# Optimization experiments

Measured on AMD Instinct MI355X. Metric: run time of the kernel, lower is better.

The kernel has to match this reference:

```python
import jax, jax.numpy as jnp
import numpy as np

B, T = 1, 1024
HIDDEN = 5376
N_HEADS = 32
N_KV = 4
HEAD_DIM = 512          # global_head_dim (full-attention layer)
ROT_DIM = 128           # head_dim * full_partial_rotary_factor (0.25)
MAX_SEQ = 4096
THETA = 1000000.0       # full_rope_theta
EPS = 1e-6


def _precompute_freqs(rot_dim, max_seq, theta, freq_base_dim):
    # freq exponent uses full head_dim (freq_base_dim) for partial rotary
    freqs = 1.0 / (theta ** (np.arange(0, rot_dim, 2, dtype=np.float32) / freq_base_dim))
    t = np.arange(max_seq, dtype=np.float32)
    ang = np.outer(t, freqs)                      # [max_seq, rot_dim//2]
    return jnp.asarray(np.cos(ang)), jnp.asarray(np.sin(ang))


def setup_inputs() -> dict:
    key = jax.random.key(0)
    ks = jax.random.split(key, 6)
    x = jax.random.normal(ks[0], (B, T, HIDDEN), jnp.float32)
    wq = jax.random.normal(ks[1], (HIDDEN, N_HEADS * HEAD_DIM), jnp.float32) * 0.02
    wk = jax.random.normal(ks[2], (HIDDEN, N_KV * HEAD_DIM), jnp.float32) * 0.02
    wo = jax.random.normal(ks[3], (N_HEADS * HEAD_DIM, HIDDEN), jnp.float32) * 0.02
    q_norm_w = 1.0 + 0.01 * jax.random.normal(ks[4], (HEAD_DIM,), jnp.float32)
    k_norm_w = 1.0 + 0.01 * jax.random.normal(ks[5], (HEAD_DIM,), jnp.float32)
    input_pos = jnp.arange(T, dtype=jnp.int32)    # prefill positions 0..T-1
    # causal mask over the full cache length: key slot s visible iff s <= query pos
    attn_mask = (jnp.arange(MAX_SEQ)[None, :] <= input_pos[:, None])[None, None]  # [1,1,T,S] bool
    fc, fs = _precompute_freqs(ROT_DIM, MAX_SEQ, THETA, HEAD_DIM)
    k_cache = jnp.zeros((B, N_KV, MAX_SEQ, HEAD_DIM), jnp.float32)
    v_cache = jnp.zeros_like(k_cache)
    return dict(x=x, input_pos=input_pos, attn_mask=attn_mask, wq=wq, wk=wk, wo=wo,
                q_norm_w=q_norm_w, k_norm_w=k_norm_w, k_cache=k_cache, v_cache=v_cache,
                freqs_cos=fc, freqs_sin=fs)


def _rmsnorm(x, w=None):
    y = x * jax.lax.rsqrt(jnp.mean(x * x, axis=-1, keepdims=True) + EPS)
    return y * w if w is not None else y


def _rope(t, cos, sin):
    # t: (B,H,T,D); rotate only the first ROT_DIM dims (interleaved pairs), pass the rest
    rot, pas = t[..., :ROT_DIM], t[..., ROT_DIM:]
    r = rot.reshape(rot.shape[:-1] + (ROT_DIM // 2, 2))
    tr, ti = r[..., 0], r[..., 1]
    c = cos[None, None]  # (1,1,T,ROT_DIM//2)
    s = sin[None, None]
    out = jnp.stack([tr * c - ti * s, tr * s + ti * c], axis=-1).reshape(rot.shape)
    return jnp.concatenate([out, pas], axis=-1)


def reference(x, input_pos, attn_mask, wq, wk, wo, q_norm_w, k_norm_w,
              k_cache, v_cache, freqs_cos, freqs_sin):
    q = (x @ wq).reshape(B, T, N_HEADS, HEAD_DIM)
    raw_k = (x @ wk).reshape(B, T, N_KV, HEAD_DIM)   # k_eq_v: raw_v = raw_k
    q = _rmsnorm(q, q_norm_w)
    k = _rmsnorm(raw_k, k_norm_w)
    v = _rmsnorm(raw_k)                               # RMSNormNoWeight on shared K=V
    q = q.transpose(0, 2, 1, 3)                       # (B,H,T,D)
    k = k.transpose(0, 2, 1, 3)
    v = v.transpose(0, 2, 1, 3)
    cos = freqs_cos[input_pos]
    sin = freqs_sin[input_pos]
    q = _rope(q, cos, sin)
    k = _rope(k, cos, sin)
    # KV cache update (index_copy along seq dim)
    k_cache = k_cache.at[:, :, input_pos, :].set(k)
    v_cache = v_cache.at[:, :, input_pos, :].set(v)
    # GQA SDPA with scale=1.0, grouped to avoid materializing repeated K/V
    G = N_HEADS // N_KV
    qg = q.reshape(B, N_KV, G, T, HEAD_DIM)
    scores = jnp.einsum('bkgtd,bksd->bkgts', qg, k_cache)
    neg = jnp.finfo(scores.dtype).min
    scores = jnp.where(attn_mask[:, :, None], scores, neg)  # (1,1,1,T,S) broadcast
    attn = jax.nn.softmax(scores, axis=-1)
    y = jnp.einsum('bkgts,bksd->bkgtd', attn, v_cache).reshape(B, N_HEADS, T, HEAD_DIM)
    y = y.transpose(0, 2, 1, 3).reshape(B, T, N_HEADS * HEAD_DIM)
    return y @ wo
```

## Files before the change

### kernel.cpp

```cpp
#include <hip/hip_runtime.h>
#include <stdint.h>

typedef unsigned short u16;
typedef _Float16 f16;
typedef f16 f16x8 __attribute__((ext_vector_type(8)));
typedef float f32x4 __attribute__((ext_vector_type(4)));
typedef unsigned short u16x4 __attribute__((ext_vector_type(4)));
typedef unsigned short u16x8 __attribute__((ext_vector_type(8)));

#define MFMA16(a, b, c) __builtin_amdgcn_mfma_f32_16x16x32_f16(a, b, c, 0, 0, 0)

__device__ __forceinline__ u16 f2h_u(float f) {
  union { f16 h; u16 u; } v; v.h = (f16)f; return v.u;
}
__device__ __forceinline__ float h2f(u16 u) {
  union { u16 u; f16 h; } v; v.u = u; return (float)v.h;
}
__device__ __forceinline__ f16x8 ld_h8(const u16* p) {
  return *(const f16x8*)p;
}
__device__ __forceinline__ void gl_lds16(const u16* g, u16* l) {
  __builtin_amdgcn_global_load_lds(
      (const __attribute__((address_space(1))) void*)g,
      (__attribute__((address_space(3))) void*)l, 16, 0, 0);
}

__global__ __launch_bounds__(256) void convert_f32_f16(
    const float* __restrict__ in, u16* __restrict__ out, int n8)
{
  int i = blockIdx.x * 256 + threadIdx.x;
  int stride = gridDim.x * 256;
  for (; i < n8; i += stride) {
    f32x4 a = *(const f32x4*)(in + (size_t)i * 8);
    f32x4 b = *(const f32x4*)(in + (size_t)i * 8 + 4);
    u16x8 o;
#pragma unroll
    for (int j = 0; j < 4; ++j) { o[j] = f2h_u(a[j]); o[4 + j] = f2h_u(b[j]); }
    *(u16x8*)(out + (size_t)i * 8) = o;
  }
}

__global__ __launch_bounds__(256) void transpose_h16(
    const u16* __restrict__ in, u16* __restrict__ out,
    int R, int C, int ldi, int ldo, long zin, long zout)
{
  __shared__ u16 tile[64 * 66];
  const u16* ip = in + (size_t)blockIdx.z * zin;
  u16* op = out + (size_t)blockIdx.z * zout;
  int x0 = blockIdx.x * 64, y0 = blockIdx.y * 64;
  int t = threadIdx.x;
  int xr = (t & 15) * 4;
  int yr = t >> 4;
#pragma unroll
  for (int p = 0; p < 4; ++p) {
    int y = yr + p * 16;
    u16x4 v = *(const u16x4*)(ip + (size_t)(y0 + y) * ldi + x0 + xr);
    tile[y * 66 + xr + 0] = v.x;
    tile[y * 66 + xr + 1] = v.y;
    tile[y * 66 + xr + 2] = v.z;
    tile[y * 66 + xr + 3] = v.w;
  }
  __syncthreads();
#pragma unroll
  for (int p = 0; p < 4; ++p) {
    int x = (t >> 4) + p * 16;
    int yq = (t & 15) * 4;
    u16x4 v;
    v.x = tile[(yq + 0) * 66 + x];
    v.y = tile[(yq + 1) * 66 + x];
    v.z = tile[(yq + 2) * 66 + x];
    v.w = tile[(yq + 3) * 66 + x];
    *(u16x4*)(op + (size_t)(x0 + x) * ldo + y0 + yq) = v;
  }
}

template <bool F32OUT>
__global__ __launch_bounds__(512, 4) void gemm_ktn(
    const u16* __restrict__ A, const float* __restrict__ W, void* __restrict__ Cv,
    int Ksp, int lda, int ldw, int ldc, long zstride)
{
  __shared__ alignas(16) u16 As[3 * 256 * 32];
  __shared__ alignas(16) u16 Bs[3 * 128 * 32];
  int tid = threadIdx.x;
  int lane = tid & 63;
  int wave = tid >> 6;
  int wm = wave >> 2, wn = wave & 3;
  int r15 = lane & 15, g = lane >> 4;

  int gx = gridDim.x, gy = gridDim.y;
  int nwg = gx * gy;
  int flat = blockIdx.y * gx + blockIdx.x;
  int q = nwg >> 3, rr = nwg & 7, xcd = flat & 7, lo = flat >> 3;
  int s = ((xcd < rr) ? xcd * (q + 1) : rr * (q + 1) + (xcd - rr) * q) + lo;
  int by = s % gy;
  int bx = s / gy;
  int row0 = by * 256, col0 = bx * 128;
  int kbeg = blockIdx.z * Ksp;

  int rA = tid >> 2;
  int pc = tid & 3;
  int cs = pc ^ ((rA >> 1) & 3);
  const u16* Ag0 = A + (size_t)(row0 + rA) * lda + kbeg + cs * 8;
  const u16* Ag1 = Ag0 + (size_t)128 * lda;

  int cB = tid & 127;
  int kc = tid >> 7;
  const float* Wg = W + (size_t)(kbeg + kc * 8) * ldw + col0 + cB;
  int bwoff = cB * 32 + ((kc ^ ((cB >> 1) & 3)) * 8);

  f32x4 acc[8][2];
#pragma unroll
  for (int i = 0; i < 8; ++i)
#pragma unroll
    for (int j = 0; j < 2; ++j) acc[i][j] = (f32x4){0.f, 0.f, 0.f, 0.f};

  int nk = Ksp >> 5;
  float bw[8];

  auto BLOAD = [&](int kk) {
#pragma unroll
    for (int j = 0; j < 8; ++j)
      bw[j] = Wg[(size_t)(kk * 32 + j) * ldw];
  };
  auto BWRITE = [&](int b) {
    u16x8 o;
#pragma unroll
    for (int j = 0; j < 8; ++j) o[j] = f2h_u(bw[j]);
    *(u16x8*)(Bs + b * 4096 + bwoff) = o;
  };
  auto STAGE_A = [&](int kk, int b) {
    u16* la = As + b * 8192 + wave * 512;
    gl_lds16(Ag0 + (size_t)kk * 32, la);
    gl_lds16(Ag1 + (size_t)kk * 32, la + 4096);
  };

  BLOAD(0);
  STAGE_A(0, 0);
  STAGE_A(1, 1);
  asm volatile("s_waitcnt vmcnt(2)" ::: "memory");
  BWRITE(0);
  asm volatile("s_waitcnt lgkmcnt(0)" ::: "memory");
  __builtin_amdgcn_s_barrier();

  int swz = (g ^ ((r15 >> 1) & 3)) * 8;
  int b0 = 0;
  for (int k = 0; k < nk; ++k) {
    const u16* Ab = As + b0 * 8192;
    const u16* Bb = Bs + b0 * 4096;
    if (k + 1 < nk) BLOAD(k + 1);
    if (k + 2 < nk) {
      int b2 = b0 + 2; if (b2 >= 3) b2 -= 3;
      STAGE_A(k + 2, b2);
    }
    f16x8 bfr[2], af[4];
#pragma unroll
    for (int ni = 0; ni < 2; ++ni)
      bfr[ni] = ld_h8(Bb + (wn * 32 + ni * 16 + r15) * 32 + swz);
#pragma unroll
    for (int m2 = 0; m2 < 4; ++m2)
      af[m2] = ld_h8(Ab + (wm * 128 + m2 * 16 + r15) * 32 + swz);
    __builtin_amdgcn_s_setprio(1);
#pragma unroll
    for (int m2 = 0; m2 < 4; ++m2)
#pragma unroll
      for (int ni = 0; ni < 2; ++ni)
        acc[m2][ni] = MFMA16(af[m2], bfr[ni], acc[m2][ni]);
    f16x8 ag[4];
#pragma unroll
    for (int m2 = 0; m2 < 4; ++m2)
      ag[m2] = ld_h8(Ab + (wm * 128 + (4 + m2) * 16 + r15) * 32 + swz);
#pragma unroll
    for (int m2 = 0; m2 < 4; ++m2)
#pragma unroll
      for (int ni = 0; ni < 2; ++ni)
        acc[4 + m2][ni] = MFMA16(ag[m2], bfr[ni], acc[4 + m2][ni]);
    __builtin_amdgcn_s_setprio(0);
    if (k + 1 < nk) {
      if (k + 2 < nk) {
        asm volatile("s_waitcnt vmcnt(2)" ::: "memory");
      } else {
        asm volatile("s_waitcnt vmcnt(0)" ::: "memory");
      }
      int b1 = b0 + 1; if (b1 >= 3) b1 -= 3;
      BWRITE(b1);
    }
    asm volatile("s_waitcnt lgkmcnt(0)" ::: "memory");
    __builtin_amdgcn_s_barrier();
    b0 = (b0 == 2) ? 0 : b0 + 1;
  }

#pragma unroll
  for (int mi = 0; mi < 8; ++mi)
#pragma unroll
    for (int ni = 0; ni < 2; ++ni) {
      int row = row0 + wm * 128 + mi * 16 + g * 4;
      int col = col0 + wn * 32 + ni * 16 + r15;
#pragma unroll
      for (int r = 0; r < 4; ++r) {
        if constexpr (F32OUT)
          ((float*)Cv)[(size_t)blockIdx.z * zstride + (size_t)(row + r) * ldc + col] = acc[mi][ni][r];
        else
          ((u16*)Cv)[(size_t)blockIdx.z * zstride + (size_t)(row + r) * ldc + col] = f2h_u(acc[mi][ni][r]);
      }
    }
}

__global__ __launch_bounds__(256) void reduce_add2_f32(
    const float* __restrict__ p, float* __restrict__ out, int n4, long half)
{
  int i = blockIdx.x * 256 + threadIdx.x;
  int stride = gridDim.x * 256;
  for (; i < n4; i += stride) {
    f32x4 a = *(const f32x4*)(p + (size_t)i * 4);
    f32x4 b = *(const f32x4*)(p + half + (size_t)i * 4);
    *(f32x4*)(out + (size_t)i * 4) = a + b;
  }
}

__global__ __launch_bounds__(256) void reduce_add4_f16(
    const float* __restrict__ p, u16* __restrict__ out, int n4, long zs)
{
  int i = blockIdx.x * 256 + threadIdx.x;
  int stride = gridDim.x * 256;
  for (; i < n4; i += stride) {
    f32x4 a = *(const f32x4*)(p + (size_t)i * 4);
    a += *(const f32x4*)(p + zs + (size_t)i * 4);
    a += *(const f32x4*)(p + 2 * zs + (size_t)i * 4);
    a += *(const f32x4*)(p + 3 * zs + (size_t)i * 4);
    u16x4 o;
#pragma unroll
    for (int j = 0; j < 4; ++j) o[j] = f2h_u(a[j]);
    *(u16x4*)(out + (size_t)i * 4) = o;
  }
}

__global__ __launch_bounds__(64) void norm_rope_q(
    u16* __restrict__ q, const float* __restrict__ w,
    const float* __restrict__ fc, const float* __restrict__ fs)
{
  int t = blockIdx.x, h = blockIdx.y, lane = threadIdx.x;
  u16* row = q + (size_t)t * 16384 + h * 512;
  u16x8 v = *(const u16x8*)(row + lane * 8);
  float x[8];
  float ss = 0.f;
#pragma unroll
  for (int j = 0; j < 8; ++j) { x[j] = h2f(v[j]); ss += x[j] * x[j]; }
#pragma unroll
  for (int m = 1; m < 64; m <<= 1) ss += __shfl_xor(ss, m, 64);
  float rms = rsqrtf(ss * (1.f / 512.f) + 1e-6f);
  f32x4 w0 = *(const f32x4*)(w + lane * 8);
  f32x4 w1 = *(const f32x4*)(w + lane * 8 + 4);
  float y[8];
#pragma unroll
  for (int j = 0; j < 4; ++j) {
    y[j] = x[j] * rms * w0[j];
    y[4 + j] = x[4 + j] * rms * w1[j];
  }
  if (lane < 16) {
    f32x4 cv = *(const f32x4*)(fc + t * 64 + lane * 4);
    f32x4 sv = *(const f32x4*)(fs + t * 64 + lane * 4);
#pragma unroll
    for (int j = 0; j < 4; ++j) {
      float c = cv[j], s = sv[j];
      float a = y[2 * j], b = y[2 * j + 1];
      y[2 * j] = a * c - b * s;
      y[2 * j + 1] = a * s + b * c;
    }
  }
  u16x8 o;
#pragma unroll
  for (int j = 0; j < 8; ++j) o[j] = f2h_u(y[j]);
  *(u16x8*)(row + lane * 8) = o;
}

__global__ __launch_bounds__(64) void norm_kv(
    u16* __restrict__ kraw, u16* __restrict__ vout, const float* __restrict__ kw,
    const float* __restrict__ fc, const float* __restrict__ fs)
{
  int t = blockIdx.x, kv = blockIdx.y, lane = threadIdx.x;
  u16* row  = kraw + (size_t)t * 2048 + kv * 512;
  u16* vrow = vout + (size_t)t * 2048 + kv * 512;
  u16x8 v = *(const u16x8*)(row + lane * 8);
  float x[8];
  float ss = 0.f;
#pragma unroll
  for (int j = 0; j < 8; ++j) { x[j] = h2f(v[j]); ss += x[j] * x[j]; }
#pragma unroll
  for (int m = 1; m < 64; m <<= 1) ss += __shfl_xor(ss, m, 64);
  float rms = rsqrtf(ss * (1.f / 512.f) + 1e-6f);
  f32x4 w0 = *(const f32x4*)(kw + lane * 8);
  f32x4 w1 = *(const f32x4*)(kw + lane * 8 + 4);
  float yk[8], yv[8];
#pragma unroll
  for (int j = 0; j < 4; ++j) {
    yv[j] = x[j] * rms;           yv[4 + j] = x[4 + j] * rms;
    yk[j] = yv[j] * w0[j];        yk[4 + j] = yv[4 + j] * w1[j];
  }
  if (lane < 16) {
    f32x4 cv = *(const f32x4*)(fc + t * 64 + lane * 4);
    f32x4 sv = *(const f32x4*)(fs + t * 64 + lane * 4);
#pragma unroll
    for (int j = 0; j < 4; ++j) {
      float c = cv[j], s = sv[j];
      float a = yk[2 * j], b = yk[2 * j + 1];
      yk[2 * j] = a * c - b * s;
      yk[2 * j + 1] = a * s + b * c;
    }
  }
  u16x8 ok, ov;
#pragma unroll
  for (int j = 0; j < 8; ++j) { ok[j] = f2h_u(yk[j]); ov[j] = f2h_u(yv[j]); }
  *(u16x8*)(row + lane * 8) = ok;
  *(u16x8*)(vrow + lane * 8) = ov;
}

__global__ __launch_bounds__(256) void attn2_kernel(
    const u16* __restrict__ Q, const u16* __restrict__ Kb,
    const u16* __restrict__ Vt, u16* __restrict__ Y)
{
  __shared__ float Sred[4 * 32 * 68];
  __shared__ u16 Plds[32 * 64];
  __shared__ float scf[32];
  __shared__ float linv[32];
  __shared__ int nf[4];

  int h = blockIdx.x;
  int qtb = 31 - blockIdx.y;
  int kv = h >> 3;
  int tid = threadIdx.x;
  int lane = tid & 63;
  int w = tid >> 6;
  int r15 = lane & 15, g = lane >> 4;
  int qbase = qtb * 32;
  int dbase = w * 128;

  int jloc = lane >> 3, cl = lane & 7;
  int jrow = w * 8 + jloc;
  int qr_sm = qbase + jrow;

  f16x8 qf[2][4];
  {
    const u16* qp = Q + (size_t)(qbase + r15) * 16384 + h * 512 + dbase + g * 8;
#pragma unroll
    for (int mi = 0; mi < 2; ++mi)
#pragma unroll
      for (int ks = 0; ks < 4; ++ks)
        qf[mi][ks] = ld_h8(qp + (size_t)mi * 16 * 16384 + ks * 32);
  }

  f32x4 acc[2][8];
#pragma unroll
  for (int mi = 0; mi < 2; ++mi)
#pragma unroll
    for (int nt = 0; nt < 8; ++nt) acc[mi][nt] = (f32x4){0.f, 0.f, 0.f, 0.f};
  float m_ = -1e30f, l_ = 0.f;

  const u16* kp_base = Kb + kv * 512 + dbase;
  const u16* vt_base = Vt + (size_t)kv * (512 * 1024) + (size_t)dbase * 1024;
  int nst = (qbase + 31) / 64 + 1;

  for (int st = 0; st < nst; ++st) {
    int s0 = st * 64;
    f32x4 sa[2][4];
#pragma unroll
    for (int mi = 0; mi < 2; ++mi)
#pragma unroll
      for (int nt = 0; nt < 4; ++nt) sa[mi][nt] = (f32x4){0.f, 0.f, 0.f, 0.f};
#pragma unroll
    for (int ks = 0; ks < 4; ++ks) {
#pragma unroll
      for (int nt = 0; nt < 4; ++nt) {
        f16x8 kf = ld_h8(kp_base + (size_t)(s0 + nt * 16 + r15) * 2048 + ks * 32 + g * 8);
#pragma unroll
        for (int mi = 0; mi < 2; ++mi)
          sa[mi][nt] = MFMA16(qf[mi][ks], kf, sa[mi][nt]);
      }
    }
    {
      float* sw = Sred + w * 32 * 68;
#pragma unroll
      for (int mi = 0; mi < 2; ++mi)
#pragma unroll
        for (int nt = 0; nt < 4; ++nt)
#pragma unroll
          for (int r = 0; r < 4; ++r)
            sw[(mi * 16 + g * 4 + r) * 68 + nt * 16 + r15] = sa[mi][nt][r];
    }
    __syncthreads();

    {
      const float* sp = Sred + jrow * 68 + cl * 8;
      f32x4 a0 = *(const f32x4*)(sp);
      f32x4 a1 = *(const f32x4*)(sp + 4);
#pragma unroll
      for (int p = 1; p < 4; ++p) {
        a0 += *(const f32x4*)(sp + p * 32 * 68);
        a1 += *(const f32x4*)(sp + p * 32 * 68 + 4);
      }
      float sv[8];
      int sbase = s0 + cl * 8;
#pragma unroll
      for (int j = 0; j < 4; ++j) {
        sv[j]     = (sbase + j     <= qr_sm) ? a0[j] : -1e30f;
        sv[4 + j] = (sbase + 4 + j <= qr_sm) ? a1[j] : -1e30f;
      }
      float mm = sv[0];
#pragma unroll
      for (int j = 1; j < 8; ++j) mm = fmaxf(mm, sv[j]);
      mm = fmaxf(mm, __shfl_xor(mm, 1, 64));
      mm = fmaxf(mm, __shfl_xor(mm, 2, 64));
      mm = fmaxf(mm, __shfl_xor(mm, 4, 64));
      bool defer = (mm <= m_ + 8.f);
      float sc;
      if (defer) { sc = 1.f; }
      else { float mn = fmaxf(m_, mm); sc = __expf(m_ - mn); m_ = mn; }
      float pv8[8], rsum = 0.f;
#pragma unroll
      for (int j = 0; j < 8; ++j) { pv8[j] = __expf(sv[j] - m_); rsum += pv8[j]; }
      rsum += __shfl_xor(rsum, 1, 64);
      rsum += __shfl_xor(rsum, 2, 64);
      rsum += __shfl_xor(rsum, 4, 64);
      l_ = l_ * sc + rsum;
      u16x8 pw;
#pragma unroll
      for (int j = 0; j < 8; ++j) pw[j] = f2h_u(pv8[j]);
      *(u16x8*)(Plds + jrow * 64 + ((cl ^ (jrow & 7)) * 8)) = pw;
      if (cl == 0) scf[jrow] = sc;
      int need = __any((int)(!defer));
      if (lane == 0) nf[w] = need;
    }
    __syncthreads();

    if (nf[0] | nf[1] | nf[2] | nf[3]) {
#pragma unroll
      for (int mi = 0; mi < 2; ++mi)
#pragma unroll
        for (int r = 0; r < 4; ++r) {
          float s = scf[mi * 16 + g * 4 + r];
#pragma unroll
          for (int nt = 0; nt < 8; ++nt) acc[mi][nt][r] *= s;
        }
    }
    f16x8 pa[2][2];
#pragma unroll
    for (int mi = 0; mi < 2; ++mi)
#pragma unroll
      for (int ks = 0; ks < 2; ++ks) {
        int row = mi * 16 + r15;
        int c = ks * 4 + g;
        pa[mi][ks] = ld_h8(Plds + row * 64 + ((c ^ (row & 7)) * 8));
      }
#pragma unroll
    for (int ks = 0; ks < 2; ++ks)
#pragma unroll
      for (int nt = 0; nt < 8; ++nt) {
        f16x8 vf = ld_h8(vt_base + (size_t)(nt * 16 + r15) * 1024 + s0 + ks * 32 + g * 8);
#pragma unroll
        for (int mi = 0; mi < 2; ++mi)
          acc[mi][nt] = MFMA16(pa[mi][ks], vf, acc[mi][nt]);
      }
  }

  if (cl == 0) linv[jrow] = 1.0f / l_;
  __syncthreads();
#pragma unroll
  for (int mi = 0; mi < 2; ++mi)
#pragma unroll
    for (int r = 0; r < 4; ++r) {
      int row = mi * 16 + g * 4 + r;
      float li = linv[row];
      u16* yp = Y + (size_t)(qbase + row) * 16384 + h * 512 + dbase + r15;
#pragma unroll
      for (int nt = 0; nt < 8; ++nt)
        yp[nt * 16] = f2h_u(acc[mi][nt][r] * li);
    }
}

extern "C" void kernel_launch(void* const* d_in, const int* in_sizes, int n_in,
                              void* d_out, int out_size, void* d_ws, size_t ws_size,
                              hipStream_t stream)
{
  const float* x  = (const float*)d_in[0];
  const float* wq = (const float*)d_in[3];
  const float* wk = (const float*)d_in[4];
  const float* wo = (const float*)d_in[5];
  const float* qw = (const float*)d_in[6];
  const float* kw = (const float*)d_in[7];
  const float* fc = (const float*)d_in[10];
  const float* fs = (const float*)d_in[11];
  float* out = (float*)d_out;
  char* ws = (char*)d_ws;

  u16* Qbuf = (u16*)(ws + 0);
  u16* Kbuf = (u16*)(ws + 33554432);
  u16* Vbuf = (u16*)(ws + 37748736);
  u16* Vt   = (u16*)(ws + 41943040);
  u16* Ybuf = (u16*)(ws + 46137344);
  u16* xh   = (u16*)(ws + 79691776);
  float* Pb  = (float*)ws;
  float* PbK = (float*)(ws + 46137344);

  convert_f32_f16<<<672, 256, 0, stream>>>(x, xh, (1024 * 5376) / 8);

  gemm_ktn<false><<<dim3(128, 4, 1), 512, 0, stream>>>(
      xh, wq, (void*)Qbuf, 5376, 5376, 16384, 16384, 0L);

  gemm_ktn<true><<<dim3(16, 4, 4), 512, 0, stream>>>(
      xh, wk, (void*)PbK, 1344, 5376, 2048, 2048, 2097152L);
  reduce_add4_f16<<<2048, 256, 0, stream>>>(PbK, Kbuf, 524288, 2097152L);

  norm_rope_q<<<dim3(1024, 32), 64, 0, stream>>>(Qbuf, qw, fc, fs);
  norm_kv<<<dim3(1024, 4), 64, 0, stream>>>(Kbuf, Vbuf, kw, fc, fs);
  transpose_h16<<<dim3(8, 16, 4), 256, 0, stream>>>(
      Vbuf, Vt, 1024, 512, 2048, 1024, 512L, 524288L);
  attn2_kernel<<<dim3(32, 32), 256, 0, stream>>>(Qbuf, Kbuf, Vt, Ybuf);

  gemm_ktn<true><<<dim3(42, 4, 2), 512, 0, stream>>>(
      Ybuf, wo, (void*)Pb, 8192, 16384, 5376, 5376, 5505024L);
  reduce_add2_f32<<<2048, 256, 0, stream>>>(Pb, out, 1376256, 5505024L);
}
```

Baseline: 853.5 us.

## Double-buffer W register prefetch two k-steps ahead in GEMM main loop

```diff
diff --git a/kernel.cpp b/kernel.cpp
--- a/kernel.cpp
+++ b/kernel.cpp
@@ -115,79 +115,126 @@
     for (int j = 0; j < 2; ++j) acc[i][j] = (f32x4){0.f, 0.f, 0.f, 0.f};
 
   int nk = Ksp >> 5;
-  float bw[8];
-
-  auto BLOAD = [&](int kk) {
-#pragma unroll
-    for (int j = 0; j < 8; ++j)
-      bw[j] = Wg[(size_t)(kk * 32 + j) * ldw];
-  };
-  auto BWRITE = [&](int b) {
-    u16x8 o;
-#pragma unroll
-    for (int j = 0; j < 8; ++j) o[j] = f2h_u(bw[j]);
-    *(u16x8*)(Bs + b * 4096 + bwoff) = o;
-  };
+  float bw0[8], bw1[8];
+
   auto STAGE_A = [&](int kk, int b) {
     u16* la = As + b * 8192 + wave * 512;
     gl_lds16(Ag0 + (size_t)kk * 32, la);
     gl_lds16(Ag1 + (size_t)kk * 32, la + 4096);
   };
-
-  BLOAD(0);
+  int swz = (g ^ ((r15 >> 1) & 3)) * 8;
+
+#define BLOAD0(kk) { _Pragma("unroll") for (int j = 0; j < 8; ++j) bw0[j] = Wg[(size_t)((kk) * 32 + j) * ldw]; }
+#define BLOAD1(kk) { _Pragma("unroll") for (int j = 0; j < 8; ++j) bw1[j] = Wg[(size_t)((kk) * 32 + j) * ldw]; }
+#define BWRITE0(b) { u16x8 o; _Pragma("unroll") for (int j = 0; j < 8; ++j) o[j] = f2h_u(bw0[j]); *(u16x8*)(Bs + (b) * 4096 + bwoff) = o; }
+#define BWRITE1(b) { u16x8 o; _Pragma("unroll") for (int j = 0; j < 8; ++j) o[j] = f2h_u(bw1[j]); *(u16x8*)(Bs + (b) * 4096 + bwoff) = o; }
+
+  BLOAD0(0);
+  BLOAD1(1);
   STAGE_A(0, 0);
   STAGE_A(1, 1);
   asm volatile("s_waitcnt vmcnt(2)" ::: "memory");
-  BWRITE(0);
+  BWRITE0(0);
   asm volatile("s_waitcnt lgkmcnt(0)" ::: "memory");
   __builtin_amdgcn_s_barrier();
 
-  int swz = (g ^ ((r15 >> 1) & 3)) * 8;
   int b0 = 0;
-  for (int k = 0; k < nk; ++k) {
-    const u16* Ab = As + b0 * 8192;
-    const u16* Bb = Bs + b0 * 4096;
-    if (k + 1 < nk) BLOAD(k + 1);
-    if (k + 2 < nk) {
-      int b2 = b0 + 2; if (b2 >= 3) b2 -= 3;
-      STAGE_A(k + 2, b2);
-    }
-    f16x8 bfr[2], af[4];
-#pragma unroll
-    for (int ni = 0; ni < 2; ++ni)
-      bfr[ni] = ld_h8(Bb + (wn * 32 + ni * 16 + r15) * 32 + swz);
-#pragma unroll
-    for (int m2 = 0; m2 < 4; ++m2)
-      af[m2] = ld_h8(Ab + (wm * 128 + m2 * 16 + r15) * 32 + swz);
-    __builtin_amdgcn_s_setprio(1);
-#pragma unroll
-    for (int m2 = 0; m2 < 4; ++m2)
+  for (int k = 0; k < nk; k += 2) {
+    {
+      const int t = k;
+      const u16* Ab = As + b0 * 8192;
+      const u16* Bb = Bs + b0 * 4096;
+      if (t + 2 < nk) {
+        BLOAD0(t + 2);
+        int b2 = b0 + 2; if (b2 >= 3) b2 -= 3;
+        STAGE_A(t + 2, b2);
+      }
+      f16x8 bfr[2], af[4];
 #pragma unroll
       for (int ni = 0; ni < 2; ++ni)
-        acc[m2][ni] = MFMA16(af[m2], bfr[ni], acc[m2][ni]);
-    f16x8 ag[4];
-#pragma unroll
-    for (int m2 = 0; m2 < 4; ++m2)
-      ag[m2] = ld_h8(Ab + (wm * 128 + (4 + m2) * 16 + r15) * 32 + swz);
-#pragma unroll
-    for (int m2 = 0; m2 < 4; ++m2)
-#pragma unroll
-      for (int ni = 0; ni < 2; ++ni)
-        acc[4 + m2][ni] = MFMA16(ag[m2], bfr[ni], acc[4 + m2][ni]);
-    __builtin_amdgcn_s_setprio(0);
-    if (k + 1 < nk) {
-      if (k + 2 < nk) {
-        asm volatile("s_waitcnt vmcnt(2)" ::: "memory");
+        bfr[ni] = ld_h8(Bb + (wn * 32 + ni * 16 + r15) * 32 + swz);
+#pragma unroll
+      for (int m2 = 0; m2 < 4; ++m2)
+        af[m2] = ld_h8(Ab + (wm * 128 + m2 * 16 + r15) * 32 + swz);
+      __builtin_amdgcn_s_setprio(1);
+#pragma unroll
+      for (int m2 = 0; m2 < 4; ++m2)
+#pragma unroll
+        for (int ni = 0; ni < 2; ++ni)
+          acc[m2][ni] = MFMA16(af[m2], bfr[ni], acc[m2][ni]);
+      f16x8 ag[4];
+#pragma unroll
+      for (int m2 = 0; m2 < 4; ++m2)
+        ag[m2] = ld_h8(Ab + (wm * 128 + (4 + m2) * 16 + r15) * 32 + swz);
+#pragma unroll
+      for (int m2 = 0; m2 < 4; ++m2)
+#pragma unroll
+        for (int ni = 0; ni < 2; ++ni)
+          acc[4 + m2][ni] = MFMA16(ag[m2], bfr[ni], acc[4 + m2][ni]);
+      __builtin_amdgcn_s_setprio(0);
+      if (t + 2 < nk) {
+        asm volatile("s_waitcnt vmcnt(10)" ::: "memory");
       } else {
         asm volatile("s_waitcnt vmcnt(0)" ::: "memory");
       }
       int b1 = b0 + 1; if (b1 >= 3) b1 -= 3;
-      BWRITE(b1);
-    }
-    asm volatile("s_waitcnt lgkmcnt(0)" ::: "memory");
-    __builtin_amdgcn_s_barrier();
-    b0 = (b0 == 2) ? 0 : b0 + 1;
-  }
+      BWRITE1(b1);
+      asm volatile("s_waitcnt lgkmcnt(0)" ::: "memory");
+      __builtin_amdgcn_s_barrier();
+      b0 = (b0 == 2) ? 0 : b0 + 1;
+    }
+    {
+      const int t = k + 1;
+      const u16* Ab = As + b0 * 8192;
+      const u16* Bb = Bs + b0 * 4096;
+      if (t + 2 < nk) {
+        BLOAD1(t + 2);
+        int b2 = b0 + 2; if (b2 >= 3) b2 -= 3;
+        STAGE_A(t + 2, b2);
+      }
+      f16x8 bfr[2], af[4];
+#pragma unroll
+      for (int ni = 0; ni < 2; ++ni)
+        bfr[ni] = ld_h8(Bb + (wn * 32 + ni * 16 + r15) * 32 + swz);
+#pragma unroll
+      for (int m2 = 0; m2 < 4; ++m2)
+        af[m2] = ld_h8(Ab + (wm * 128 + m2 * 16 + r15) * 32 + swz);
+      __builtin_amdgcn_s_setprio(1);
+#pragma unroll
+      for (int m2 = 0; m2 < 4; ++m2)
+#pragma unroll
+        for (int ni = 0; ni < 2; ++ni)
+          acc[m2][ni] = MFMA16(af[m2], bfr[ni], acc[m2][ni]);
+      f16x8 ag[4];
+#pragma unroll
+      for (int m2 = 0; m2 < 4; ++m2)
+        ag[m2] = ld_h8(Ab + (wm * 128 + (4 + m2) * 16 + r15) * 32 + swz);
+#pragma unroll
+      for (int m2 = 0; m2 < 4; ++m2)
+#pragma unroll
+        for (int ni = 0; ni < 2; ++ni)
+          acc[4 + m2][ni] = MFMA16(ag[m2], bfr[ni], acc[4 + m2][ni]);
+      __builtin_amdgcn_s_setprio(0);
+      if (t + 1 < nk) {
+        if (t + 2 < nk) {
+          asm volatile("s_waitcnt vmcnt(10)" ::: "memory");
+        } else {
+          asm volatile("s_waitcnt vmcnt(0)" ::: "memory");
+        }
+        int b1 = b0 + 1; if (b1 >= 3) b1 -= 3;
+        BWRITE0(b1);
+      } else {
+        asm volatile("s_waitcnt vmcnt(0)" ::: "memory");
+      }
+      asm volatile("s_waitcnt lgkmcnt(0)" ::: "memory");
+      __builtin_amdgcn_s_barrier();
+      b0 = (b0 == 2) ? 0 : b0 + 1;
+    }
+  }
+#undef BLOAD0
+#undef BLOAD1
+#undef BWRITE0
+#undef BWRITE1
 
 #pragma unroll
   for (int mi = 0; mi < 8; ++mi)
```

Result: slower. 3.151 ms (+269.2%).
